# Performance work log

Hardware: AMD Instinct MI355X
Metric: run time of the kernel (lower is better)

The kernel has to match this reference:

```python
import jax, jax.numpy as jnp
import numpy as np

N, MUL, NUM_ELEM = 2048, 128, 10
D_IN = 9                      # single-copy input irreps 0e+1o+2e -> 1+3+5
IN_DIMS = (1, 3, 5)           # per-irrep dims of irreps_in
OUT_DIMS = (1, 3)             # per-irrep dims of irreps_out (0e, 1o)
OUT_SLICES = ((0, 1), (1, 4)) # slices into per-mul output of width 4
# (nu, out_idx, n_basis) entries, mirroring reduced_symmetric_tensor_product_basis
ENTRIES = ((1, 0, 1), (1, 1, 1), (2, 0, 3), (2, 1, 2), (3, 0, 4), (3, 1, 2))


def setup_inputs() -> dict:
    key = jax.random.key(0)
    ks = jax.random.split(key, 2 + 2 * len(ENTRIES))
    inp = {}
    inp["node_feats"] = jax.random.normal(ks[0], (N, MUL * D_IN), dtype=jnp.float32)
    inp["species"] = jax.random.randint(ks[1], (N,), 0, NUM_ELEM)
    for i, (nu, oi, nb) in enumerate(ENTRIES):
        d = OUT_DIMS[oi]
        inp[f"basis{i}"] = jax.random.normal(ks[2 + 2 * i], (D_IN,) * nu + (nb, d), dtype=jnp.float32)
        inp[f"weight{i}"] = jax.random.normal(ks[3 + 2 * i], (NUM_ELEM, nb, MUL), dtype=jnp.float32) * (1.0 / np.sqrt(nb))
    return inp


def _to_per_mul(x):
    # (N, sum mul*dim) -> (N, mul, 9)
    pieces, off = [], 0
    for d in IN_DIMS:
        pieces.append(x[:, off:off + MUL * d].reshape(-1, MUL, d))
        off += MUL * d
    return jnp.concatenate(pieces, axis=-1)


def _from_per_mul(x):
    # (N, mul, 4) -> (N, mul*1 + mul*3)
    pieces = []
    for oi, d in enumerate(OUT_DIMS):
        lo, hi = OUT_SLICES[oi]
        pieces.append(x[:, :, lo:hi].reshape(-1, MUL * d))
    return jnp.concatenate(pieces, axis=-1)


def _forward(node_feats, bases, weights, species):
    feats = _to_per_mul(node_feats)                         # (N, mul, 9)
    out = jnp.zeros((feats.shape[0], MUL, 4), dtype=feats.dtype)
    for i, (nu, oi, nb) in enumerate(ENTRIES):
        basis = jax.lax.stop_gradient(bases[i]).astype(feats.dtype)
        tmp = jnp.einsum('a...,nma->nm...', basis, feats)   # (N, mul, 9^(nu-1), nb, d)
        for _ in range(nu - 1):
            tmp = jnp.einsum('nma...,nma->nm...', tmp, feats)
        w = weights[i][species]                             # (N, nb, mul) per-species gather
        contracted = jnp.einsum('nsm,nmsp->nmp', w, tmp)    # (N, mul, d)
        lo, hi = OUT_SLICES[oi]
        out = out.at[:, :, lo:hi].add(contracted)
    return _from_per_mul(out)


def reference(node_feats, species, basis0, weight0, basis1, weight1, basis2, weight2,
              basis3, weight3, basis4, weight4, basis5, weight5):
    bases = [basis0, basis1, basis2, basis3, basis4, basis5]
    weights = [weight0, weight1, weight2, weight3, weight4, weight5]
    return _forward(node_feats, bases, weights, species)
```

## Files before the change

### kernel.cpp

```cpp
#include <hip/hip_runtime.h>


#define N_NODES 2048
#define MUL     128
#define NROW    1152
#define NQ      45
#define NC      165
#define Q4_BASE 12
#define C4_BASE 147
#define S4_TOTAL 642

__global__ void k_prep(const float* __restrict__ b0, const float* __restrict__ b1,
                       const float* __restrict__ b2, const float* __restrict__ b3,
                       const float* __restrict__ b4, const float* __restrict__ b5,
                       float4* __restrict__ S) {
    const int t = threadIdx.x;
    if (t < 9) {
        S[t] = make_float4(b0[t], b1[t * 3 + 0], b1[t * 3 + 1], b1[t * 3 + 2]);
    } else if (t < Q4_BASE) {
        S[t] = make_float4(0.f, 0.f, 0.f, 0.f);
    } else if (t < Q4_BASE + NQ) {
        const int k = t - Q4_BASE;
        int a = -1, b = -1, kk = k;
        for (int aa = 0; aa < 9 && a < 0; ++aa) {
            const int cnt = 9 - aa;
            if (kk < cnt) { a = aa; b = aa + kk; } else kk -= cnt;
        }
        const float mult = (a == b) ? 0.5f : 1.0f;
        const int i1 = a * 9 + b, i2 = b * 9 + a;
        float s2[3], s3[6];
        for (int s = 0; s < 3; ++s)
            s2[s] = (b2[i1 * 3 + s] + b2[i2 * 3 + s]) * mult;
        for (int s = 0; s < 2; ++s)
            for (int d = 0; d < 3; ++d)
                s3[s * 3 + d] = (b3[(i1 * 2 + s) * 3 + d] + b3[(i2 * 2 + s) * 3 + d]) * mult;
        S[Q4_BASE + k * 3 + 0] = make_float4(s2[0], s2[1], s2[2], 0.f);
        S[Q4_BASE + k * 3 + 1] = make_float4(s3[0], s3[1], s3[2], s3[3]);
        S[Q4_BASE + k * 3 + 2] = make_float4(s3[4], s3[5], 0.f, 0.f);
    } else if (t < Q4_BASE + NQ + NC) {
        const int k = t - Q4_BASE - NQ;
        int a = -1, b = -1, c = -1, kk = k;
        for (int aa = 0; aa < 9 && a < 0; ++aa)
            for (int bb = aa; bb < 9 && a < 0; ++bb) {
                const int cnt = 9 - bb;
                if (kk < cnt) { a = aa; b = bb; c = bb + kk; } else kk -= cnt;
            }
        const float mult = (a == b && b == c) ? (1.0f / 6.0f)
                         : ((a == b || b == c) ? 0.5f : 1.0f);
        int p[6];
        p[0] = (a * 9 + b) * 9 + c;  p[1] = (a * 9 + c) * 9 + b;
        p[2] = (b * 9 + a) * 9 + c;  p[3] = (b * 9 + c) * 9 + a;
        p[4] = (c * 9 + a) * 9 + b;  p[5] = (c * 9 + b) * 9 + a;
        float s4[4], s5[6];
        for (int s = 0; s < 4; ++s) {
            float v = 0.f;
            for (int j = 0; j < 6; ++j) v += b4[p[j] * 4 + s];
            s4[s] = v * mult;
        }
        for (int s = 0; s < 2; ++s)
            for (int d = 0; d < 3; ++d) {
                float v = 0.f;
                for (int j = 0; j < 6; ++j) v += b5[(p[j] * 2 + s) * 3 + d];
                s5[s * 3 + d] = v * mult;
            }
        S[C4_BASE + k * 3 + 0] = make_float4(s4[0], s4[1], s4[2], s4[3]);
        S[C4_BASE + k * 3 + 1] = make_float4(s5[0], s5[1], s5[2], s5[3]);
        S[C4_BASE + k * 3 + 2] = make_float4(s5[4], s5[5], 0.f, 0.f);
    }
}

typedef float fvec4 __attribute__((ext_vector_type(4)));

__global__ __launch_bounds__(256) void k_eval(
        const float* __restrict__ nf, const int* __restrict__ species,
        const float* __restrict__ w0, const float* __restrict__ w1,
        const float* __restrict__ w2, const float* __restrict__ w3,
        const float* __restrict__ w4, const float* __restrict__ w5,
        const float* __restrict__ Sg, float* __restrict__ out) {
#if defined(__HIP_DEVICE_COMPILE__)
    typedef const __attribute__((address_space(4))) fvec4* S4cp;
    S4cp S = (S4cp)(unsigned long long)Sg;

    const int tid = threadIdx.x;
    const int m = tid & 127;
    const int n = blockIdx.x * 2 + (tid >> 7);

    const float* __restrict__ row = nf + (size_t)n * NROW;
    float f[9];
    f[0] = row[m];
#pragma unroll
    for (int j = 0; j < 3; ++j) f[1 + j] = row[128 + 3 * m + j];
#pragma unroll
    for (int j = 0; j < 5; ++j) f[4 + j] = row[512 + 5 * m + j];

    const int e = species[n];
    const float wv0 = w0[e * MUL + m];
    const float wv1 = w1[e * MUL + m];
    float wv2[3], wv3[2], wv4[4], wv5[2];
#pragma unroll
    for (int s = 0; s < 3; ++s) wv2[s] = w2[(e * 3 + s) * MUL + m];
#pragma unroll
    for (int s = 0; s < 2; ++s) wv3[s] = w3[(e * 2 + s) * MUL + m];
#pragma unroll
    for (int s = 0; s < 4; ++s) wv4[s] = w4[(e * 4 + s) * MUL + m];
#pragma unroll
    for (int s = 0; s < 2; ++s) wv5[s] = w5[(e * 2 + s) * MUL + m];

    float A0 = 0.f;
    float A1[3] = {};
    float B2[3] = {}, B3[6] = {};
    float B4[4] = {}, B5[6] = {};

#pragma unroll
    for (int a = 0; a < 9; ++a) {
        const fvec4 L = S[a];
        A0    += L.x * f[a];
        A1[0] += L.y * f[a];
        A1[1] += L.z * f[a];
        A1[2] += L.w * f[a];
    }

    int kq = 0, kc = 0;
#pragma unroll
    for (int a = 0; a < 9; ++a) {
#pragma unroll
        for (int b = a; b < 9; ++b) {
            const float q = f[a] * f[b];
            {
                const fvec4 r0 = S[Q4_BASE + kq * 3 + 0];
                const fvec4 r1 = S[Q4_BASE + kq * 3 + 1];
                const fvec4 r2 = S[Q4_BASE + kq * 3 + 2];
                B2[0] += q * r0.x; B2[1] += q * r0.y; B2[2] += q * r0.z;
                B3[0] += q * r1.x; B3[1] += q * r1.y; B3[2] += q * r1.z;
                B3[3] += q * r1.w; B3[4] += q * r2.x; B3[5] += q * r2.y;
                ++kq;
            }
#pragma unroll
            for (int c = b; c < 9; ++c) {
                const fvec4 r0 = S[C4_BASE + kc * 3 + 0];
                const fvec4 r1 = S[C4_BASE + kc * 3 + 1];
                const fvec4 r2 = S[C4_BASE + kc * 3 + 2];
                const float tt = q * f[c];
                B4[0] += tt * r0.x; B4[1] += tt * r0.y;
                B4[2] += tt * r0.z; B4[3] += tt * r0.w;
                B5[0] += tt * r1.x; B5[1] += tt * r1.y; B5[2] += tt * r1.z;
                B5[3] += tt * r1.w; B5[4] += tt * r2.x; B5[5] += tt * r2.y;
                ++kc;
            }
        }
    }

    float* __restrict__ orow = out + (size_t)n * 512;
    orow[m] = wv0 * A0
            + wv2[0] * B2[0] + wv2[1] * B2[1] + wv2[2] * B2[2]
            + wv4[0] * B4[0] + wv4[1] * B4[1] + wv4[2] * B4[2] + wv4[3] * B4[3];
#pragma unroll
    for (int d = 0; d < 3; ++d) {
        orow[128 + 3 * m + d] = wv1 * A1[d]
                              + wv3[0] * B3[d] + wv3[1] * B3[3 + d]
                              + wv5[0] * B5[d] + wv5[1] * B5[3 + d];
    }
#endif
}

extern "C" void kernel_launch(void* const* d_in, const int* in_sizes, int n_in,
                              void* d_out, int out_size, void* d_ws, size_t ws_size,
                              hipStream_t stream) {
    const float* nf      = (const float*)d_in[0];
    const int*   species = (const int*)d_in[1];
    const float* b0 = (const float*)d_in[2];  const float* w0 = (const float*)d_in[3];
    const float* b1 = (const float*)d_in[4];  const float* w1 = (const float*)d_in[5];
    const float* b2 = (const float*)d_in[6];  const float* w2 = (const float*)d_in[7];
    const float* b3 = (const float*)d_in[8];  const float* w3 = (const float*)d_in[9];
    const float* b4 = (const float*)d_in[10]; const float* w4 = (const float*)d_in[11];
    const float* b5 = (const float*)d_in[12]; const float* w5 = (const float*)d_in[13];
    float* out = (float*)d_out;

    float4* S = (float4*)d_ws;

    hipLaunchKernelGGL(k_prep, dim3(1), dim3(256), 0, stream,
                       b0, b1, b2, b3, b4, b5, S);
    hipLaunchKernelGGL(k_eval, dim3(1024), dim3(256), 0, stream,
                       nf, species, w0, w1, w2, w3, w4, w5,
                       (const float*)S, out);
}
```

Measured before the change: 114.0 us.

## Split per-node cubic contraction across two half-blocks with shared-memory reduction

Each block now handles one node instead of two. The two 128-thread halves split the work: one half does the linear, quadratic and first part of the cubic terms, the other does the rest of the cubic terms. The second half's partial sums go through shared memory and a barrier before the first half applies the weights and writes the output. The aim is to double the thread count and balance per-thread FLOPs for more parallelism and shorter critical paths. In exchange it adds a __syncthreads, LDS traffic, a second read of node features by both halves, and a tighter launch bound (256, 8) that may cause register spills.

```diff
diff --git a/kernel.cpp b/kernel.cpp
--- a/kernel.cpp
+++ b/kernel.cpp
@@ -6,6 +6,7 @@
 #define NROW    1152
 #define NQ      45
 #define NC      165
+#define KSPLIT  57
 #define Q4_BASE 12
 #define C4_BASE 147
 #define S4_TOTAL 642
@@ -71,7 +72,7 @@
 
 typedef float fvec4 __attribute__((ext_vector_type(4)));
 
-__global__ __launch_bounds__(256) void k_eval(
+__global__ __launch_bounds__(256, 8) void k_eval(
         const float* __restrict__ nf, const int* __restrict__ species,
         const float* __restrict__ w0, const float* __restrict__ w1,
         const float* __restrict__ w2, const float* __restrict__ w3,
@@ -81,9 +82,12 @@
     typedef const __attribute__((address_space(4))) fvec4* S4cp;
     S4cp S = (S4cp)(unsigned long long)Sg;
 
+    __shared__ float red[MUL * 12];
+
     const int tid = threadIdx.x;
     const int m = tid & 127;
-    const int n = blockIdx.x * 2 + (tid >> 7);
+    const int half = tid >> 7;
+    const int n = blockIdx.x;
 
     const float* __restrict__ row = nf + (size_t)n * NROW;
     float f[9];
@@ -93,72 +97,112 @@
 #pragma unroll
     for (int j = 0; j < 5; ++j) f[4 + j] = row[512 + 5 * m + j];
 
-    const int e = species[n];
-    const float wv0 = w0[e * MUL + m];
-    const float wv1 = w1[e * MUL + m];
-    float wv2[3], wv3[2], wv4[4], wv5[2];
-#pragma unroll
-    for (int s = 0; s < 3; ++s) wv2[s] = w2[(e * 3 + s) * MUL + m];
-#pragma unroll
-    for (int s = 0; s < 2; ++s) wv3[s] = w3[(e * 2 + s) * MUL + m];
-#pragma unroll
-    for (int s = 0; s < 4; ++s) wv4[s] = w4[(e * 4 + s) * MUL + m];
-#pragma unroll
-    for (int s = 0; s < 2; ++s) wv5[s] = w5[(e * 2 + s) * MUL + m];
-
-    float A0 = 0.f;
-    float A1[3] = {};
+    float A0 = 0.f, A1[3] = {};
     float B2[3] = {}, B3[6] = {};
     float B4[4] = {}, B5[6] = {};
 
-#pragma unroll
-    for (int a = 0; a < 9; ++a) {
-        const fvec4 L = S[a];
-        A0    += L.x * f[a];
-        A1[0] += L.y * f[a];
-        A1[1] += L.z * f[a];
-        A1[2] += L.w * f[a];
+    if (half == 1) {
+        int kc = 0;
+#pragma unroll
+        for (int a = 0; a < 9; ++a) {
+#pragma unroll
+            for (int b = a; b < 9; ++b) {
+                const float q = f[a] * f[b];
+#pragma unroll
+                for (int c = b; c < 9; ++c) {
+                    if (kc >= KSPLIT) {
+                        const fvec4 r0 = S[C4_BASE + kc * 3 + 0];
+                        const fvec4 r1 = S[C4_BASE + kc * 3 + 1];
+                        const fvec4 r2 = S[C4_BASE + kc * 3 + 2];
+                        const float tt = q * f[c];
+                        B4[0] += tt * r0.x; B4[1] += tt * r0.y;
+                        B4[2] += tt * r0.z; B4[3] += tt * r0.w;
+                        B5[0] += tt * r1.x; B5[1] += tt * r1.y; B5[2] += tt * r1.z;
+                        B5[3] += tt * r1.w; B5[4] += tt * r2.x; B5[5] += tt * r2.y;
+                    }
+                    ++kc;
+                }
+            }
+        }
+        float* __restrict__ dst = &red[m * 12];
+#pragma unroll
+        for (int j = 0; j < 4; ++j) dst[j] = B4[j];
+#pragma unroll
+        for (int j = 0; j < 6; ++j) dst[4 + j] = B5[j];
+    } else {
+#pragma unroll
+        for (int a = 0; a < 9; ++a) {
+            const fvec4 L = S[a];
+            A0    += L.x * f[a];
+            A1[0] += L.y * f[a];
+            A1[1] += L.z * f[a];
+            A1[2] += L.w * f[a];
+        }
+        int kq = 0, kc = 0;
+#pragma unroll
+        for (int a = 0; a < 9; ++a) {
+#pragma unroll
+            for (int b = a; b < 9; ++b) {
+                const float q = f[a] * f[b];
+                {
+                    const fvec4 r0 = S[Q4_BASE + kq * 3 + 0];
+                    const fvec4 r1 = S[Q4_BASE + kq * 3 + 1];
+                    const fvec4 r2 = S[Q4_BASE + kq * 3 + 2];
+                    B2[0] += q * r0.x; B2[1] += q * r0.y; B2[2] += q * r0.z;
+                    B3[0] += q * r1.x; B3[1] += q * r1.y; B3[2] += q * r1.z;
+                    B3[3] += q * r1.w; B3[4] += q * r2.x; B3[5] += q * r2.y;
+                    ++kq;
+                }
+#pragma unroll
+                for (int c = b; c < 9; ++c) {
+                    if (kc < KSPLIT) {
+                        const fvec4 r0 = S[C4_BASE + kc * 3 + 0];
+                        const fvec4 r1 = S[C4_BASE + kc * 3 + 1];
+                        const fvec4 r2 = S[C4_BASE + kc * 3 + 2];
+                        const float tt = q * f[c];
+                        B4[0] += tt * r0.x; B4[1] += tt * r0.y;
+                        B4[2] += tt * r0.z; B4[3] += tt * r0.w;
+                        B5[0] += tt * r1.x; B5[1] += tt * r1.y; B5[2] += tt * r1.z;
+                        B5[3] += tt * r1.w; B5[4] += tt * r2.x; B5[5] += tt * r2.y;
+                    }
+                    ++kc;
+                }
+            }
+        }
     }
 
-    int kq = 0, kc = 0;
-#pragma unroll
-    for (int a = 0; a < 9; ++a) {
-#pragma unroll
-        for (int b = a; b < 9; ++b) {
-            const float q = f[a] * f[b];
-            {
-                const fvec4 r0 = S[Q4_BASE + kq * 3 + 0];
-                const fvec4 r1 = S[Q4_BASE + kq * 3 + 1];
-                const fvec4 r2 = S[Q4_BASE + kq * 3 + 2];
-                B2[0] += q * r0.x; B2[1] += q * r0.y; B2[2] += q * r0.z;
-                B3[0] += q * r1.x; B3[1] += q * r1.y; B3[2] += q * r1.z;
-                B3[3] += q * r1.w; B3[4] += q * r2.x; B3[5] += q * r2.y;
-                ++kq;
-            }
-#pragma unroll
-            for (int c = b; c < 9; ++c) {
-                const fvec4 r0 = S[C4_BASE + kc * 3 + 0];
-                const fvec4 r1 = S[C4_BASE + kc * 3 + 1];
-                const fvec4 r2 = S[C4_BASE + kc * 3 + 2];
-                const float tt = q * f[c];
-                B4[0] += tt * r0.x; B4[1] += tt * r0.y;
-                B4[2] += tt * r0.z; B4[3] += tt * r0.w;
-                B5[0] += tt * r1.x; B5[1] += tt * r1.y; B5[2] += tt * r1.z;
-                B5[3] += tt * r1.w; B5[4] += tt * r2.x; B5[5] += tt * r2.y;
-                ++kc;
-            }
-        }
-    }
-
-    float* __restrict__ orow = out + (size_t)n * 512;
-    orow[m] = wv0 * A0
-            + wv2[0] * B2[0] + wv2[1] * B2[1] + wv2[2] * B2[2]
-            + wv4[0] * B4[0] + wv4[1] * B4[1] + wv4[2] * B4[2] + wv4[3] * B4[3];
-#pragma unroll
-    for (int d = 0; d < 3; ++d) {
-        orow[128 + 3 * m + d] = wv1 * A1[d]
-                              + wv3[0] * B3[d] + wv3[1] * B3[3 + d]
-                              + wv5[0] * B5[d] + wv5[1] * B5[3 + d];
+    __syncthreads();
+
+    if (half == 0) {
+        const float* __restrict__ src = &red[m * 12];
+#pragma unroll
+        for (int j = 0; j < 4; ++j) B4[j] += src[j];
+#pragma unroll
+        for (int j = 0; j < 6; ++j) B5[j] += src[4 + j];
+
+        const int e = species[n];
+        const float wv0 = w0[e * MUL + m];
+        const float wv1 = w1[e * MUL + m];
+        float wv2[3], wv3[2], wv4[4], wv5[2];
+#pragma unroll
+        for (int s = 0; s < 3; ++s) wv2[s] = w2[(e * 3 + s) * MUL + m];
+#pragma unroll
+        for (int s = 0; s < 2; ++s) wv3[s] = w3[(e * 2 + s) * MUL + m];
+#pragma unroll
+        for (int s = 0; s < 4; ++s) wv4[s] = w4[(e * 4 + s) * MUL + m];
+#pragma unroll
+        for (int s = 0; s < 2; ++s) wv5[s] = w5[(e * 2 + s) * MUL + m];
+
+        float* __restrict__ orow = out + (size_t)n * 512;
+        orow[m] = wv0 * A0
+                + wv2[0] * B2[0] + wv2[1] * B2[1] + wv2[2] * B2[2]
+                + wv4[0] * B4[0] + wv4[1] * B4[1] + wv4[2] * B4[2] + wv4[3] * B4[3];
+#pragma unroll
+        for (int d = 0; d < 3; ++d) {
+            orow[128 + 3 * m + d] = wv1 * A1[d]
+                                  + wv3[0] * B3[d] + wv3[1] * B3[3 + d]
+                                  + wv5[0] * B5[d] + wv5[1] * B5[3 + d];
+        }
     }
 #endif
 }
@@ -180,7 +224,7 @@
 
     hipLaunchKernelGGL(k_prep, dim3(1), dim3(256), 0, stream,
                        b0, b1, b2, b3, b4, b5, S);
-    hipLaunchKernelGGL(k_eval, dim3(1024), dim3(256), 0, stream,
+    hipLaunchKernelGGL(k_eval, dim3(N_NODES), dim3(256), 0, stream,
                        nf, species, w0, w1, w2, w3, w4, w5,
                        (const float*)S, out);
 }
```

Result: faster. 109.6 us (-3.9%).
